# Performance work log

Hardware: AMD Instinct MI355X
Metric: run time of the kernel (lower is better)

Reference implementation:

```python
import jax, jax.numpy as jnp
import numpy as np

N_NODES = 100000
IN_CH = 128
HID = 256
EMB = 128
N_EDGES_GRAPH = 1000000
N_PAIRS = 500000
BN_EPS = 1e-5


def setup_inputs() -> dict:
    key = jax.random.key(0)
    ks = jax.random.split(key, 20)
    glorot = lambda k, fi, fo: jax.random.normal(k, (fi, fo), jnp.float32) * (1.0 / np.sqrt(fi))
    pair_dim = EMB * 4 + 2  # 514
    return {
        "x": jax.random.normal(ks[0], (N_NODES, IN_CH), jnp.float32),
        "edge_index": jax.random.randint(ks[1], (2, N_EDGES_GRAPH), 0, N_NODES, jnp.int64),
        "edge_pairs": jax.random.randint(ks[2], (N_PAIRS, 2), 0, N_NODES, jnp.int64),
        # normalizer buffers
        "x_mean": jnp.zeros((IN_CH,), jnp.float32),
        "x_std": jnp.ones((IN_CH,), jnp.float32),
        # log-degree buffer (as after set_degree)
        "log_degree": jax.random.uniform(ks[3], (N_NODES,), jnp.float32) * 5.0,
        # encoder: Linear(in,hid) -> BN(hid) -> ReLU -> Dropout -> Linear(hid,emb) -> ReLU
        "W1": glorot(ks[4], IN_CH, HID), "b1": jnp.zeros((HID,), jnp.float32),
        "bn_gamma": jnp.ones((HID,), jnp.float32), "bn_beta": jnp.zeros((HID,), jnp.float32),
        "bn_mean": jnp.zeros((HID,), jnp.float32), "bn_var": jnp.ones((HID,), jnp.float32),
        "W2": glorot(ks[5], HID, EMB), "b2": jnp.zeros((EMB,), jnp.float32),
        # scorer: Linear(514,256) -> ReLU -> Dropout -> Linear(256,128) -> ReLU -> Linear(128,1)
        "SW1": glorot(ks[6], pair_dim, HID), "Sb1": jnp.zeros((HID,), jnp.float32),
        "SW2": glorot(ks[7], HID, HID // 2), "Sb2": jnp.zeros((HID // 2,), jnp.float32),
        "SW3": glorot(ks[8], HID // 2, 1), "Sb3": jnp.zeros((1,), jnp.float32),
    }


def reference(x, edge_index, edge_pairs, x_mean, x_std, log_degree,
              W1, b1, bn_gamma, bn_beta, bn_mean, bn_var, W2, b2,
              SW1, Sb1, SW2, Sb2, SW3, Sb3):
    # ---- encode ----
    xf = jnp.nan_to_num(x, nan=0.0, posinf=0.0, neginf=0.0)
    xf = jnp.clip((xf - x_mean) / x_std, -10.0, 10.0)
    h = xf @ W1 + b1                                    # [N, HID]
    h = (h - bn_mean) * jax.lax.rsqrt(bn_var + BN_EPS) * bn_gamma + bn_beta  # BN (eval)
    h = jax.nn.relu(h)                                  # dropout = identity (eval)
    z = jax.nn.relu(h @ W2 + b2)                        # [N, EMB]
    # ---- score_from_embeddings ----
    si = edge_pairs[:, 0]
    di = edge_pairs[:, 1]
    src = z[si]                                         # [E, EMB]
    dst = z[di]
    deg_pair = jnp.stack([log_degree[si], log_degree[di]], axis=1)  # [E, 2]
    pair = jnp.concatenate([src, dst, src * dst, jnp.abs(src - dst), deg_pair], axis=1)  # [E, 4*EMB+2]
    s = jax.nn.relu(pair @ SW1 + Sb1)
    s = jax.nn.relu(s @ SW2 + Sb2)
    logits = (s @ SW3 + Sb3).reshape(-1)                # [E]
    return jnp.nan_to_num(logits, nan=0.0, posinf=20.0, neginf=-20.0)
```

## Files before the change

kernel.cpp:

```cpp
#include <hip/hip_runtime.h>
#include <hip/hip_bf16.h>
#include <math.h>

typedef unsigned short u16;
typedef __attribute__((ext_vector_type(8))) short bf16x8;
typedef __attribute__((ext_vector_type(8))) unsigned short u16x8;
typedef __attribute__((ext_vector_type(4))) float f32x4;
typedef __attribute__((ext_vector_type(4))) unsigned u32x4;
typedef __attribute__((ext_vector_type(2))) unsigned u32x2;

#define N_NODES 100000
#define IN_CH 128
#define HID 256
#define EMB 128
#define N_PAIRS 500000
#define BN_EPS 1e-5f

#define PBM 64

__device__ __forceinline__ u16 f2bf(float f) {
    unsigned u = __builtin_bit_cast(unsigned, f);
    unsigned r = u + 0x7FFFu + ((u >> 16) & 1u);
    return (u16)(r >> 16);
}
__device__ __forceinline__ float bf2f(u16 h) {
    unsigned u = ((unsigned)h) << 16;
    return __builtin_bit_cast(float, u);
}
__device__ __forceinline__ unsigned pk2(float a, float b) {
    __hip_bfloat162 h = __float22bfloat162_rn(make_float2(a, b));
    unsigned u;
    __builtin_memcpy(&u, &h, sizeof(u));
    return u;
}

__device__ __forceinline__ void store8(u16* buf, int base, const float* v) {
    u32x4 hv;
    #pragma unroll
    for (int q = 0; q < 4; ++q) hv[q] = pk2(v[2 * q], v[2 * q + 1]);
    *reinterpret_cast<u32x4*>(&buf[base]) = hv;
}

__global__ __launch_bounds__(256) void prep_weights(
    const float* __restrict__ SW1, const float* __restrict__ SW2,
    const float* __restrict__ W1,  const float* __restrict__ W2,
    u16* __restrict__ w1h, u16* __restrict__ w2h,
    u16* __restrict__ w1nh, u16* __restrict__ w1nl,
    u16* __restrict__ w2nh, u16* __restrict__ w2nl)
{
    const int tid = blockIdx.x * 256 + threadIdx.x;
    if (tid < 131072) {
        const int j = tid & 7, l = (tid >> 3) & 63, ks = (tid >> 9) & 15, mt = tid >> 13;
        const int n = mt * 16 + (l & 15);
        const int k = ks * 32 + ((l >> 4) << 3) + j;
        w1h[tid] = f2bf(SW1[(size_t)k * HID + n]);
    } else if (tid < 163840) {
        const int t2 = tid - 131072;
        const int j = t2 & 7, l = (t2 >> 3) & 63, ks = (t2 >> 9) & 7, mt = t2 >> 12;
        const int n = mt * 16 + (l & 15);
        const int k = ks * 32 + ((l >> 4) << 3) + j;
        w2h[t2] = f2bf(SW2[(size_t)k * (HID / 2) + n]);
    } else if (tid < 196608) {
        const int t3 = tid - 163840;
        const int j = t3 & 7, l = (t3 >> 3) & 63, ks = (t3 >> 9) & 3, mt = t3 >> 11;
        const int n = mt * 16 + (l & 15);
        const int k = ks * 32 + ((l >> 4) << 3) + j;
        const float v = W1[(size_t)k * HID + n];
        const u16 h = f2bf(v);
        w1nh[t3] = h;
        w1nl[t3] = f2bf(v - bf2f(h));
    } else if (tid < 229376) {
        const int t4 = tid - 196608;
        const int j = t4 & 7, l = (t4 >> 3) & 63, ks = (t4 >> 9) & 7, mt = t4 >> 12;
        const int n = mt * 16 + (l & 15);
        const int k = ks * 32 + ((l >> 4) << 3) + j;
        const float v = W2[(size_t)k * EMB + n];
        const u16 h = f2bf(v);
        w2nh[t4] = h;
        w2nl[t4] = f2bf(v - bf2f(h));
    }
}

__global__ __launch_bounds__(256) void node_mfma_kernel(
    const float* __restrict__ x,
    const float* __restrict__ x_mean, const float* __restrict__ x_std,
    const float* __restrict__ b1,
    const float* __restrict__ bn_gamma, const float* __restrict__ bn_beta,
    const float* __restrict__ bn_mean,  const float* __restrict__ bn_var,
    const float* __restrict__ b2,
    const u16* __restrict__ w1nh, const u16* __restrict__ w1nl,
    const u16* __restrict__ w2nh, const u16* __restrict__ w2nl,
    u16* __restrict__ z)
{
    __shared__ __align__(16) u16 XF[8192];
    __shared__ __align__(16) u16 HF[16384];

    const int t   = threadIdx.x;
    const int w   = t >> 6;
    const int l   = t & 63;
    const int l15 = l & 15;
    const int l4  = l >> 4;
    const int n0  = blockIdx.x * 64;
    const int nd  = (n0 + l < N_NODES) ? (n0 + l) : (N_NODES - 1);

    {
        const float* xp = x + (size_t)nd * IN_CH + w * 32;
        float v[32];
        #pragma unroll
        for (int q = 0; q < 8; ++q)
            *reinterpret_cast<float4*>(&v[q * 4]) = *reinterpret_cast<const float4*>(xp + q * 4);
        #pragma unroll
        for (int q = 0; q < 8; ++q) {
            float4 m4 = *reinterpret_cast<const float4*>(x_mean + w * 32 + q * 4);
            float4 s4 = *reinterpret_cast<const float4*>(x_std  + w * 32 + q * 4);
            float mm[4] = {m4.x, m4.y, m4.z, m4.w};
            float ss[4] = {s4.x, s4.y, s4.z, s4.w};
            #pragma unroll
            for (int e = 0; e < 4; ++e) {
                float val = v[q * 4 + e];
                if (!isfinite(val)) val = 0.0f;
                val = (val - mm[e]) / ss[e];
                v[q * 4 + e] = fminf(fmaxf(val, -10.0f), 10.0f);
            }
        }
        #pragma unroll
        for (int q = 0; q < 4; ++q) {
            const int base = (w * 4 + l4) * 512 + (l15 + 16 * q) * 8;
            store8(XF, base, &v[q * 8]);
        }
    }
    __syncthreads();

    f32x4 acc[4][4];
    #pragma unroll
    for (int m = 0; m < 4; ++m)
        #pragma unroll
        for (int nt = 0; nt < 4; ++nt) acc[m][nt] = (f32x4){0.f, 0.f, 0.f, 0.f};

    #pragma unroll
    for (int sl = 0; sl < 4; ++sl) {
        bf16x8 wh[4], wl[4];
        #pragma unroll
        for (int m = 0; m < 4; ++m) {
            const size_t bo = ((size_t)((w * 4 + m) * 4 + sl) * 64 + l) * 8;
            wh[m] = *reinterpret_cast<const bf16x8*>(&w1nh[bo]);
            wl[m] = *reinterpret_cast<const bf16x8*>(&w1nl[bo]);
        }
        bf16x8 fh[4];
        #pragma unroll
        for (int nt = 0; nt < 4; ++nt)
            fh[nt] = *reinterpret_cast<const bf16x8*>(&XF[(sl * 4 + nt) * 512 + l * 8]);
        __builtin_amdgcn_s_setprio(1);
        #pragma unroll
        for (int m = 0; m < 4; ++m)
            #pragma unroll
            for (int nt = 0; nt < 4; ++nt)
                acc[m][nt] = __builtin_amdgcn_mfma_f32_16x16x32_bf16(wh[m], fh[nt], acc[m][nt], 0, 0, 0);
        #pragma unroll
        for (int m = 0; m < 4; ++m)
            #pragma unroll
            for (int nt = 0; nt < 4; ++nt)
                acc[m][nt] = __builtin_amdgcn_mfma_f32_16x16x32_bf16(wl[m], fh[nt], acc[m][nt], 0, 0, 0);
        __builtin_amdgcn_s_setprio(0);
    }

    #pragma unroll
    for (int m = 0; m < 4; ++m) {
        const int mt = w * 4 + m;
        const int nb = mt * 16 + l4 * 4;
        float4 b1v = *reinterpret_cast<const float4*>(b1 + nb);
        float4 gv  = *reinterpret_cast<const float4*>(bn_gamma + nb);
        float4 bev = *reinterpret_cast<const float4*>(bn_beta + nb);
        float4 mev = *reinterpret_cast<const float4*>(bn_mean + nb);
        float4 vav = *reinterpret_cast<const float4*>(bn_var + nb);
        float scale[4], shift[4];
        float bb[4] = {b1v.x, b1v.y, b1v.z, b1v.w};
        float gg[4] = {gv.x, gv.y, gv.z, gv.w};
        float be[4] = {bev.x, bev.y, bev.z, bev.w};
        float me[4] = {mev.x, mev.y, mev.z, mev.w};
        float va[4] = {vav.x, vav.y, vav.z, vav.w};
        #pragma unroll
        for (int r = 0; r < 4; ++r) {
            scale[r] = gg[r] * rsqrtf(va[r] + BN_EPS);
            shift[r] = (bb[r] - me[r]) * scale[r] + be[r];
        }
        #pragma unroll
        for (int nt = 0; nt < 4; ++nt) {
            float v[4];
            #pragma unroll
            for (int r = 0; r < 4; ++r)
                v[r] = fmaxf(fmaf(acc[m][nt][r], scale[r], shift[r]), 0.0f);
            u32x2 hv;
            hv[0] = pk2(v[0], v[1]);
            hv[1] = pk2(v[2], v[3]);
            const int base = ((mt >> 1) * 4 + nt) * 512
                           + (l15 + 16 * ((mt & 1) * 2 + (l4 >> 1))) * 8
                           + (l4 & 1) * 4;
            *reinterpret_cast<u32x2*>(&HF[base]) = hv;
        }
    }
    __syncthreads();

    f32x4 acc2[2][4];
    #pragma unroll
    for (int m2 = 0; m2 < 2; ++m2)
        #pragma unroll
        for (int nt = 0; nt < 4; ++nt) acc2[m2][nt] = (f32x4){0.f, 0.f, 0.f, 0.f};

    #pragma unroll
    for (int ks2 = 0; ks2 < 8; ++ks2) {
        bf16x8 wh2[2], wl2[2];
        #pragma unroll
        for (int m2 = 0; m2 < 2; ++m2) {
            const size_t bo = ((size_t)((w * 2 + m2) * 8 + ks2) * 64 + l) * 8;
            wh2[m2] = *reinterpret_cast<const bf16x8*>(&w2nh[bo]);
            wl2[m2] = *reinterpret_cast<const bf16x8*>(&w2nl[bo]);
        }
        bf16x8 fh[4];
        #pragma unroll
        for (int nt = 0; nt < 4; ++nt)
            fh[nt] = *reinterpret_cast<const bf16x8*>(&HF[(ks2 * 4 + nt) * 512 + l * 8]);
        __builtin_amdgcn_s_setprio(1);
        #pragma unroll
        for (int m2 = 0; m2 < 2; ++m2)
            #pragma unroll
            for (int nt = 0; nt < 4; ++nt)
                acc2[m2][nt] = __builtin_amdgcn_mfma_f32_16x16x32_bf16(wh2[m2], fh[nt], acc2[m2][nt], 0, 0, 0);
        #pragma unroll
        for (int m2 = 0; m2 < 2; ++m2)
            #pragma unroll
            for (int nt = 0; nt < 4; ++nt)
                acc2[m2][nt] = __builtin_amdgcn_mfma_f32_16x16x32_bf16(wl2[m2], fh[nt], acc2[m2][nt], 0, 0, 0);
        __builtin_amdgcn_s_setprio(0);
    }

    #pragma unroll
    for (int m2 = 0; m2 < 2; ++m2) {
        const int nb2 = (w * 2 + m2) * 16 + l4 * 4;
        float4 b2v = *reinterpret_cast<const float4*>(b2 + nb2);
        float bb[4] = {b2v.x, b2v.y, b2v.z, b2v.w};
        #pragma unroll
        for (int nt = 0; nt < 4; ++nt) {
            const int node = n0 + nt * 16 + l15;
            if (node < N_NODES) {
                float v0 = fmaxf(acc2[m2][nt][0] + bb[0], 0.0f);
                float v1 = fmaxf(acc2[m2][nt][1] + bb[1], 0.0f);
                float v2 = fmaxf(acc2[m2][nt][2] + bb[2], 0.0f);
                float v3 = fmaxf(acc2[m2][nt][3] + bb[3], 0.0f);
                u32x2 hv;
                hv[0] = pk2(v0, v1);
                hv[1] = pk2(v2, v3);
                *reinterpret_cast<u32x2*>(z + (size_t)node * EMB + nb2) = hv;
            }
        }
    }
}

__global__ __launch_bounds__(256) void pair_mfma_kernel(
    const u16* __restrict__ z,
    const int* __restrict__ pairs,
    const float* __restrict__ logdeg,
    const u16* __restrict__ w1h,
    const u16* __restrict__ w2h,
    const float* __restrict__ SW1, const float* __restrict__ Sb1,
    const float* __restrict__ Sb2,
    const float* __restrict__ SW3, const float* __restrict__ Sb3,
    float* __restrict__ out)
{
    __shared__ __align__(16) u16 F0[8192];
    __shared__ __align__(16) u16 F1[8192];
    __shared__ __align__(16) u16 F2[8192];
    __shared__ __align__(16) u16 F3[8192];
    __shared__ float red[4][4][16];

    const int t   = threadIdx.x;
    const int w   = t >> 6;
    const int l   = t & 63;
    const int l15 = l & 15;
    const int l4  = l >> 4;
    const int p0  = blockIdx.x * PBM;

    const int qb  = (w & 1) * 2;
    const int bS0 = (((w >> 1)) * 4 + l4) * 512 + (l15 + 16 * (qb + 0)) * 8;
    const int bS1 = (((w >> 1)) * 4 + l4) * 512 + (l15 + 16 * (qb + 1)) * 8;
    const int bD0 = ((2 + (w >> 1)) * 4 + l4) * 512 + (l15 + 16 * (qb + 0)) * 8;
    const int bD1 = ((2 + (w >> 1)) * 4 + l4) * 512 + (l15 + 16 * (qb + 1)) * 8;

    const int gp  = (p0 + l < N_PAIRS) ? (p0 + l) : (N_PAIRS - 1);
    const int gsi = pairs[(size_t)gp * 2 + 0];
    const int gdi = pairs[(size_t)gp * 2 + 1];

    const u16* zs0 = z + (size_t)gsi * EMB + w * 16;
    const u16* zd0 = z + (size_t)gdi * EMB + w * 16;
    u16x8 s00 = *reinterpret_cast<const u16x8*>(zs0);
    u16x8 s01 = *reinterpret_cast<const u16x8*>(zs0 + 8);
    u16x8 d00 = *reinterpret_cast<const u16x8*>(zd0);
    u16x8 d01 = *reinterpret_cast<const u16x8*>(zd0 + 8);
    u16x8 s10 = *reinterpret_cast<const u16x8*>(zs0 + 64);
    u16x8 s11 = *reinterpret_cast<const u16x8*>(zs0 + 72);
    u16x8 d10 = *reinterpret_cast<const u16x8*>(zd0 + 64);
    u16x8 d11 = *reinterpret_cast<const u16x8*>(zd0 + 72);

    auto rebuildR = [&](u16x8 sa, u16x8 sb, u16x8 da, u16x8 db, float* pv, float* av) {
        #pragma unroll
        for (int qq = 0; qq < 8; ++qq) {
            const float s = bf2f(sa[qq]);
            const float d = bf2f(da[qq]);
            pv[qq] = s * d;
            av[qq] = fabsf(s - d);
        }
        #pragma unroll
        for (int qq = 0; qq < 8; ++qq) {
            const float s = bf2f(sb[qq]);
            const float d = bf2f(db[qq]);
            pv[8 + qq] = s * d;
            av[8 + qq] = fabsf(s - d);
        }
    };

    *reinterpret_cast<u16x8*>(&F0[bS0]) = s00;
    *reinterpret_cast<u16x8*>(&F0[bS1]) = s01;
    *reinterpret_cast<u16x8*>(&F0[bD0]) = d00;
    *reinterpret_cast<u16x8*>(&F0[bD1]) = d01;
    *reinterpret_cast<u16x8*>(&F1[bS0]) = s10;
    *reinterpret_cast<u16x8*>(&F1[bS1]) = s11;
    *reinterpret_cast<u16x8*>(&F1[bD0]) = d10;
    *reinterpret_cast<u16x8*>(&F1[bD1]) = d11;
    {
        float pv[16], av[16];
        rebuildR(s00, s01, d00, d01, pv, av);
        store8(F2, bS0, pv + 0);
        store8(F2, bS1, pv + 8);
        store8(F2, bD0, av + 0);
        store8(F2, bD1, av + 8);
        rebuildR(s10, s11, d10, d11, pv, av);
        store8(F3, bS0, pv + 0);
        store8(F3, bS1, pv + 8);
        store8(F3, bD0, av + 0);
        store8(F3, bD1, av + 8);
    }

    float ldS[4], ldD[4];
    #pragma unroll
    for (int nt = 0; nt < 4; ++nt) {
        const int pidx = (p0 + nt * 16 + l15 < N_PAIRS) ? (p0 + nt * 16 + l15) : (N_PAIRS - 1);
        ldS[nt] = logdeg[pairs[(size_t)pidx * 2 + 0]];
        ldD[nt] = logdeg[pairs[(size_t)pidx * 2 + 1]];
    }

    __syncthreads();

    f32x4 acc[4][4];
    #pragma unroll
    for (int m = 0; m < 4; ++m)
        #pragma unroll
        for (int nt = 0; nt < 4; ++nt) acc[m][nt] = (f32x4){0.f, 0.f, 0.f, 0.f};

    auto run_pass = [&](const u16* buf, int k0, int k1, int k2, int k3) {
        const int ksg[4] = {k0, k1, k2, k3};
        bf16x8 wh[2][4];
        #pragma unroll
        for (int m = 0; m < 4; ++m) {
            const size_t bo = ((size_t)((w * 4 + m) * 16 + ksg[0]) * 64 + l) * 8;
            wh[0][m] = *reinterpret_cast<const bf16x8*>(&w1h[bo]);
        }
        #pragma unroll
        for (int sl = 0; sl < 4; ++sl) {
            const int cur = sl & 1;
            if (sl < 3) {
                #pragma unroll
                for (int m = 0; m < 4; ++m) {
                    const size_t bo = ((size_t)((w * 4 + m) * 16 + ksg[sl + 1]) * 64 + l) * 8;
                    wh[cur ^ 1][m] = *reinterpret_cast<const bf16x8*>(&w1h[bo]);
                }
            }
            #pragma unroll
            for (int nh = 0; nh < 2; ++nh) {
                bf16x8 fh[2];
                #pragma unroll
                for (int e = 0; e < 2; ++e)
                    fh[e] = *reinterpret_cast<const bf16x8*>(&buf[(sl * 4 + nh * 2 + e) * 512 + l * 8]);
                __builtin_amdgcn_s_setprio(1);
                #pragma unroll
                for (int m = 0; m < 4; ++m)
                    #pragma unroll
                    for (int e = 0; e < 2; ++e)
                        acc[m][nh * 2 + e] = __builtin_amdgcn_mfma_f32_16x16x32_bf16(wh[cur][m], fh[e], acc[m][nh * 2 + e], 0, 0, 0);
                __builtin_amdgcn_s_setprio(0);
            }
        }
    };

    run_pass(F0, 0, 1, 4, 5);
    run_pass(F2, 8, 9, 12, 13);
    run_pass(F1, 2, 3, 6, 7);
    run_pass(F3, 10, 11, 14, 15);
    __syncthreads();

    f32x4 acc2[2][4];
    #pragma unroll
    for (int m2 = 0; m2 < 2; ++m2)
        #pragma unroll
        for (int nt = 0; nt < 4; ++nt) acc2[m2][nt] = (f32x4){0.f, 0.f, 0.f, 0.f};

    auto epi1 = [&](u16* buf, int g) {
        #pragma unroll
        for (int mm = 0; mm < 2; ++mm) {
            const int m  = 2 * g + mm;
            const int mt = w * 4 + m;
            const int nb = mt * 16 + l4 * 4;
            float sb[4], wa[4], wb[4];
            *reinterpret_cast<float4*>(sb) = *reinterpret_cast<const float4*>(&Sb1[nb]);
            *reinterpret_cast<float4*>(wa) = *reinterpret_cast<const float4*>(&SW1[(size_t)512 * HID + nb]);
            *reinterpret_cast<float4*>(wb) = *reinterpret_cast<const float4*>(&SW1[(size_t)513 * HID + nb]);
            #pragma unroll
            for (int nt = 0; nt < 4; ++nt) {
                float v[4];
                #pragma unroll
                for (int r = 0; r < 4; ++r) {
                    float x0 = acc[m][nt][r] + sb[r];
                    x0 = fmaf(ldS[nt], wa[r], x0);
                    x0 = fmaf(ldD[nt], wb[r], x0);
                    v[r] = fmaxf(x0, 0.0f);
                }
                u32x2 hv;
                hv[0] = pk2(v[0], v[1]);
                hv[1] = pk2(v[2], v[3]);
                const int base = (w * 4 + nt) * 512
                               + (l15 + 16 * ((m & 1) * 2 + (l4 >> 1))) * 8
                               + (l4 & 1) * 4;
                *reinterpret_cast<u32x2*>(&buf[base]) = hv;
            }
        }
    };

    auto mfma2 = [&](const u16* buf, int g) {
        #pragma unroll
        for (int cs = 0; cs < 4; ++cs) {
            const int ks2 = cs * 2 + g;
            bf16x8 wh2[2];
            #pragma unroll
            for (int m2 = 0; m2 < 2; ++m2) {
                const size_t bo = ((size_t)((w * 2 + m2) * 8 + ks2) * 64 + l) * 8;
                wh2[m2] = *reinterpret_cast<const bf16x8*>(&w2h[bo]);
            }
            #pragma unroll
            for (int nh = 0; nh < 2; ++nh) {
                bf16x8 fh[2];
                #pragma unroll
                for (int e = 0; e < 2; ++e)
                    fh[e] = *reinterpret_cast<const bf16x8*>(&buf[(cs * 4 + nh * 2 + e) * 512 + l * 8]);
                __builtin_amdgcn_s_setprio(1);
                #pragma unroll
                for (int m2 = 0; m2 < 2; ++m2)
                    #pragma unroll
                    for (int e = 0; e < 2; ++e)
                        acc2[m2][nh * 2 + e] = __builtin_amdgcn_mfma_f32_16x16x32_bf16(wh2[m2], fh[e], acc2[m2][nh * 2 + e], 0, 0, 0);
                __builtin_amdgcn_s_setprio(0);
            }
        }
    };

    epi1(F0, 0);
    __syncthreads();
    epi1(F1, 1);
    mfma2(F0, 0);
    __syncthreads();
    mfma2(F1, 1);

    {
        float part[4] = {0.f, 0.f, 0.f, 0.f};
        #pragma unroll
        for (int m2 = 0; m2 < 2; ++m2) {
            const int nb2 = (w * 2 + m2) * 16 + l4 * 4;
            float sb[4], w3[4];
            *reinterpret_cast<float4*>(sb) = *reinterpret_cast<const float4*>(&Sb2[nb2]);
            *reinterpret_cast<float4*>(w3) = *reinterpret_cast<const float4*>(&SW3[nb2]);
            #pragma unroll
            for (int nt = 0; nt < 4; ++nt)
                #pragma unroll
                for (int r = 0; r < 4; ++r)
                    part[nt] = fmaf(fmaxf(acc2[m2][nt][r] + sb[r], 0.0f), w3[r], part[nt]);
        }
        #pragma unroll
        for (int nt = 0; nt < 4; ++nt) {
            part[nt] += __shfl_xor(part[nt], 16);
            part[nt] += __shfl_xor(part[nt], 32);
        }
        if (l < 16) {
            #pragma unroll
            for (int nt = 0; nt < 4; ++nt) red[w][nt][l15] = part[nt];
        }
    }
    __syncthreads();

    if (t < 64) {
        const int nt = t >> 4, pp = t & 15;
        float v = red[0][nt][pp] + red[1][nt][pp] + red[2][nt][pp] + red[3][nt][pp] + Sb3[0];
        if (isnan(v)) v = 0.0f;
        else if (isinf(v)) v = (v > 0.0f) ? 20.0f : -20.0f;
        const int pidx = p0 + nt * 16 + pp;
        if (pidx < N_PAIRS) out[pidx] = v;
    }
}

extern "C" void kernel_launch(void* const* d_in, const int* in_sizes, int n_in,
                              void* d_out, int out_size, void* d_ws, size_t ws_size,
                              hipStream_t stream)
{
    const float* x        = (const float*)d_in[0];
    const int*   pairs    = (const int*)d_in[2];
    const float* x_mean   = (const float*)d_in[3];
    const float* x_std    = (const float*)d_in[4];
    const float* logdeg   = (const float*)d_in[5];
    const float* W1       = (const float*)d_in[6];
    const float* b1       = (const float*)d_in[7];
    const float* bn_gamma = (const float*)d_in[8];
    const float* bn_beta  = (const float*)d_in[9];
    const float* bn_mean  = (const float*)d_in[10];
    const float* bn_var   = (const float*)d_in[11];
    const float* W2       = (const float*)d_in[12];
    const float* b2       = (const float*)d_in[13];
    const float* SW1      = (const float*)d_in[14];
    const float* Sb1      = (const float*)d_in[15];
    const float* SW2      = (const float*)d_in[16];
    const float* Sb2      = (const float*)d_in[17];
    const float* SW3      = (const float*)d_in[18];
    const float* Sb3      = (const float*)d_in[19];

    float* outp = (float*)d_out;

    char* wsb = (char*)d_ws;
    u16* zbuf = (u16*)wsb;
    u16* w1h  = (u16*)(wsb + 25600000);
    u16* w2h  = (u16*)(wsb + 25862144);
    u16* w1nh = (u16*)(wsb + 25927680);
    u16* w1nl = (u16*)(wsb + 25993216);
    u16* w2nh = (u16*)(wsb + 26058752);
    u16* w2nl = (u16*)(wsb + 26124288);

    prep_weights<<<896, 256, 0, stream>>>(SW1, SW2, W1, W2,
                                          w1h, w2h,
                                          w1nh, w1nl, w2nh, w2nl);

    node_mfma_kernel<<<(N_NODES + 63) / 64, 256, 0, stream>>>(
        x, x_mean, x_std, b1, bn_gamma, bn_beta, bn_mean, bn_var, b2,
        w1nh, w1nl, w2nh, w2nl, zbuf);

    pair_mfma_kernel<<<(N_PAIRS + PBM - 1) / PBM, 256, 0, stream>>>(
        zbuf, pairs, logdeg, w1h, w2h, SW1, Sb1, Sb2, SW3, Sb3, outp);
}
```

Measured before the change: 248.0 us.

## Switch scorer first layer to 32x32x16 MFMA tiles with matching layouts

Replaces the 16x16x32 bf16 MFMA tiling of the first scorer layer with 32x32x16 MFMA. The SW1 prepacking, the LDS feature layout, the log-degree loads and the epilogue write-back are all remapped to the 32-wide fragment layout. The larger tiles mean fewer MFMA instructions and fewer weight and feature fragment loads per FLOP. The cost is bigger accumulator vectors and more complex index mapping, which raises register pressure and the risk of layout bugs.

```diff
diff --git a/kernel.cpp b/kernel.cpp
--- a/kernel.cpp
+++ b/kernel.cpp
@@ -6,6 +6,7 @@
 typedef __attribute__((ext_vector_type(8))) short bf16x8;
 typedef __attribute__((ext_vector_type(8))) unsigned short u16x8;
 typedef __attribute__((ext_vector_type(4))) float f32x4;
+typedef __attribute__((ext_vector_type(16))) float f32x16;
 typedef __attribute__((ext_vector_type(4))) unsigned u32x4;
 typedef __attribute__((ext_vector_type(2))) unsigned u32x2;
 
@@ -50,9 +51,9 @@
 {
     const int tid = blockIdx.x * 256 + threadIdx.x;
     if (tid < 131072) {
-        const int j = tid & 7, l = (tid >> 3) & 63, ks = (tid >> 9) & 15, mt = tid >> 13;
-        const int n = mt * 16 + (l & 15);
-        const int k = ks * 32 + ((l >> 4) << 3) + j;
+        const int j = tid & 7, l = (tid >> 3) & 63, ks16 = (tid >> 9) & 31, mt32 = tid >> 14;
+        const int n = mt32 * 32 + (l & 31);
+        const int k = ks16 * 16 + ((l >> 5) << 3) + j;
         w1h[tid] = f2bf(SW1[(size_t)k * HID + n]);
     } else if (tid < 163840) {
         const int t2 = tid - 131072;
@@ -278,13 +279,15 @@
     const int l   = t & 63;
     const int l15 = l & 15;
     const int l4  = l >> 4;
+    const int hi5 = l >> 5;
+    const int l31 = l & 31;
     const int p0  = blockIdx.x * PBM;
 
-    const int qb  = (w & 1) * 2;
-    const int bS0 = (((w >> 1)) * 4 + l4) * 512 + (l15 + 16 * (qb + 0)) * 8;
-    const int bS1 = (((w >> 1)) * 4 + l4) * 512 + (l15 + 16 * (qb + 1)) * 8;
-    const int bD0 = ((2 + (w >> 1)) * 4 + l4) * 512 + (l15 + 16 * (qb + 0)) * 8;
-    const int bD1 = ((2 + (w >> 1)) * 4 + l4) * 512 + (l15 + 16 * (qb + 1)) * 8;
+    const int nw  = l >> 5;
+    const int sB0 = ((w * 2 + nw) * 64 + l31) * 8;
+    const int sB1 = sB0 + 32 * 8;
+    const int dB0 = (((4 + w) * 2 + nw) * 64 + l31) * 8;
+    const int dB1 = dB0 + 32 * 8;
 
     const int gp  = (p0 + l < N_PAIRS) ? (p0 + l) : (N_PAIRS - 1);
     const int gsi = pairs[(size_t)gp * 2 + 0];
@@ -318,83 +321,82 @@
         }
     };
 
-    *reinterpret_cast<u16x8*>(&F0[bS0]) = s00;
-    *reinterpret_cast<u16x8*>(&F0[bS1]) = s01;
-    *reinterpret_cast<u16x8*>(&F0[bD0]) = d00;
-    *reinterpret_cast<u16x8*>(&F0[bD1]) = d01;
-    *reinterpret_cast<u16x8*>(&F1[bS0]) = s10;
-    *reinterpret_cast<u16x8*>(&F1[bS1]) = s11;
-    *reinterpret_cast<u16x8*>(&F1[bD0]) = d10;
-    *reinterpret_cast<u16x8*>(&F1[bD1]) = d11;
+    *reinterpret_cast<u16x8*>(&F0[sB0]) = s00;
+    *reinterpret_cast<u16x8*>(&F0[sB1]) = s01;
+    *reinterpret_cast<u16x8*>(&F0[dB0]) = d00;
+    *reinterpret_cast<u16x8*>(&F0[dB1]) = d01;
+    *reinterpret_cast<u16x8*>(&F1[sB0]) = s10;
+    *reinterpret_cast<u16x8*>(&F1[sB1]) = s11;
+    *reinterpret_cast<u16x8*>(&F1[dB0]) = d10;
+    *reinterpret_cast<u16x8*>(&F1[dB1]) = d11;
     {
         float pv[16], av[16];
         rebuildR(s00, s01, d00, d01, pv, av);
-        store8(F2, bS0, pv + 0);
-        store8(F2, bS1, pv + 8);
-        store8(F2, bD0, av + 0);
-        store8(F2, bD1, av + 8);
+        store8(F2, sB0, pv + 0);
+        store8(F2, sB1, pv + 8);
+        store8(F2, dB0, av + 0);
+        store8(F2, dB1, av + 8);
         rebuildR(s10, s11, d10, d11, pv, av);
-        store8(F3, bS0, pv + 0);
-        store8(F3, bS1, pv + 8);
-        store8(F3, bD0, av + 0);
-        store8(F3, bD1, av + 8);
-    }
-
-    float ldS[4], ldD[4];
-    #pragma unroll
-    for (int nt = 0; nt < 4; ++nt) {
-        const int pidx = (p0 + nt * 16 + l15 < N_PAIRS) ? (p0 + nt * 16 + l15) : (N_PAIRS - 1);
-        ldS[nt] = logdeg[pairs[(size_t)pidx * 2 + 0]];
-        ldD[nt] = logdeg[pairs[(size_t)pidx * 2 + 1]];
-    }
-
-    __syncthreads();
-
-    f32x4 acc[4][4];
-    #pragma unroll
-    for (int m = 0; m < 4; ++m)
-        #pragma unroll
-        for (int nt = 0; nt < 4; ++nt) acc[m][nt] = (f32x4){0.f, 0.f, 0.f, 0.f};
-
-    auto run_pass = [&](const u16* buf, int k0, int k1, int k2, int k3) {
-        const int ksg[4] = {k0, k1, k2, k3};
-        bf16x8 wh[2][4];
-        #pragma unroll
-        for (int m = 0; m < 4; ++m) {
-            const size_t bo = ((size_t)((w * 4 + m) * 16 + ksg[0]) * 64 + l) * 8;
-            wh[0][m] = *reinterpret_cast<const bf16x8*>(&w1h[bo]);
-        }
-        #pragma unroll
-        for (int sl = 0; sl < 4; ++sl) {
-            const int cur = sl & 1;
-            if (sl < 3) {
+        store8(F3, sB0, pv + 0);
+        store8(F3, sB1, pv + 8);
+        store8(F3, dB0, av + 0);
+        store8(F3, dB1, av + 8);
+    }
+
+    float ldS2[2], ldD2[2];
+    #pragma unroll
+    for (int g2 = 0; g2 < 2; ++g2) {
+        const int pidx = (p0 + g2 * 32 + l31 < N_PAIRS) ? (p0 + g2 * 32 + l31) : (N_PAIRS - 1);
+        ldS2[g2] = logdeg[pairs[(size_t)pidx * 2 + 0]];
+        ldD2[g2] = logdeg[pairs[(size_t)pidx * 2 + 1]];
+    }
+
+    __syncthreads();
+
+    f32x16 acc32[2][2];
+    #pragma unroll
+    for (int mi = 0; mi < 2; ++mi)
+        #pragma unroll
+        for (int nt = 0; nt < 2; ++nt)
+            #pragma unroll
+            for (int r = 0; r < 16; ++r) acc32[mi][nt][r] = 0.0f;
+
+    auto run_pass32 = [&](const u16* buf, int kA, int kB) {
+        bf16x8 wh[2][2];
+        #pragma unroll
+        for (int mi = 0; mi < 2; ++mi) {
+            const size_t bo = ((size_t)((2 * w + mi) * 32 + kA) * 64 + l) * 8;
+            wh[0][mi] = *reinterpret_cast<const bf16x8*>(&w1h[bo]);
+        }
+        #pragma unroll
+        for (int ksl = 0; ksl < 8; ++ksl) {
+            const int cur = ksl & 1;
+            if (ksl < 7) {
+                const int gks = (ksl + 1 < 4) ? (kA + ksl + 1) : (kB + ksl - 3);
                 #pragma unroll
-                for (int m = 0; m < 4; ++m) {
-                    const size_t bo = ((size_t)((w * 4 + m) * 16 + ksg[sl + 1]) * 64 + l) * 8;
-                    wh[cur ^ 1][m] = *reinterpret_cast<const bf16x8*>(&w1h[bo]);
+                for (int mi = 0; mi < 2; ++mi) {
+                    const size_t bo = ((size_t)((2 * w + mi) * 32 + gks) * 64 + l) * 8;
+                    wh[cur ^ 1][mi] = *reinterpret_cast<const bf16x8*>(&w1h[bo]);
                 }
             }
-            #pragma unroll
-            for (int nh = 0; nh < 2; ++nh) {
-                bf16x8 fh[2];
+            bf16x8 fh[2];
+            #pragma unroll
+            for (int nt = 0; nt < 2; ++nt)
+                fh[nt] = *reinterpret_cast<const bf16x8*>(&buf[((ksl * 2 + nt) * 64 + l) * 8]);
+            __builtin_amdgcn_s_setprio(1);
+            #pragma unroll
+            for (int mi = 0; mi < 2; ++mi)
                 #pragma unroll
-                for (int e = 0; e < 2; ++e)
-                    fh[e] = *reinterpret_cast<const bf16x8*>(&buf[(sl * 4 + nh * 2 + e) * 512 + l * 8]);
-                __builtin_amdgcn_s_setprio(1);
-                #pragma unroll
-                for (int m = 0; m < 4; ++m)
-                    #pragma unroll
-                    for (int e = 0; e < 2; ++e)
-                        acc[m][nh * 2 + e] = __builtin_amdgcn_mfma_f32_16x16x32_bf16(wh[cur][m], fh[e], acc[m][nh * 2 + e], 0, 0, 0);
-                __builtin_amdgcn_s_setprio(0);
-            }
+                for (int nt = 0; nt < 2; ++nt)
+                    acc32[mi][nt] = __builtin_amdgcn_mfma_f32_32x32x16_bf16(wh[cur][mi], fh[nt], acc32[mi][nt], 0, 0, 0);
+            __builtin_amdgcn_s_setprio(0);
         }
     };
 
-    run_pass(F0, 0, 1, 4, 5);
-    run_pass(F2, 8, 9, 12, 13);
-    run_pass(F1, 2, 3, 6, 7);
-    run_pass(F3, 10, 11, 14, 15);
+    run_pass32(F0, 0, 8);
+    run_pass32(F2, 16, 24);
+    run_pass32(F1, 4, 12);
+    run_pass32(F3, 20, 28);
     __syncthreads();
 
     f32x4 acc2[2][4];
@@ -403,32 +405,32 @@
         #pragma unroll
         for (int nt = 0; nt < 4; ++nt) acc2[m2][nt] = (f32x4){0.f, 0.f, 0.f, 0.f};
 
-    auto epi1 = [&](u16* buf, int g) {
-        #pragma unroll
-        for (int mm = 0; mm < 2; ++mm) {
-            const int m  = 2 * g + mm;
-            const int mt = w * 4 + m;
-            const int nb = mt * 16 + l4 * 4;
-            float sb[4], wa[4], wb[4];
-            *reinterpret_cast<float4*>(sb) = *reinterpret_cast<const float4*>(&Sb1[nb]);
-            *reinterpret_cast<float4*>(wa) = *reinterpret_cast<const float4*>(&SW1[(size_t)512 * HID + nb]);
-            *reinterpret_cast<float4*>(wb) = *reinterpret_cast<const float4*>(&SW1[(size_t)513 * HID + nb]);
-            #pragma unroll
-            for (int nt = 0; nt < 4; ++nt) {
+    auto epi1_32 = [&](u16* buf, int mi) {
+        const int mt32 = 2 * w + mi;
+        #pragma unroll
+        for (int nt = 0; nt < 2; ++nt) {
+            const float lS = ldS2[nt];
+            const float lD = ldD2[nt];
+            const int nt2 = nt * 2 + ((l >> 4) & 1);
+            #pragma unroll
+            for (int q = 0; q < 4; ++q) {
+                const int nb = mt32 * 32 + 8 * q + 4 * hi5;
+                float sb[4], wa[4], wb[4];
+                *reinterpret_cast<float4*>(sb) = *reinterpret_cast<const float4*>(&Sb1[nb]);
+                *reinterpret_cast<float4*>(wa) = *reinterpret_cast<const float4*>(&SW1[(size_t)512 * HID + nb]);
+                *reinterpret_cast<float4*>(wb) = *reinterpret_cast<const float4*>(&SW1[(size_t)513 * HID + nb]);
                 float v[4];
                 #pragma unroll
-                for (int r = 0; r < 4; ++r) {
-                    float x0 = acc[m][nt][r] + sb[r];
-                    x0 = fmaf(ldS[nt], wa[r], x0);
-                    x0 = fmaf(ldD[nt], wb[r], x0);
-                    v[r] = fmaxf(x0, 0.0f);
+                for (int rr = 0; rr < 4; ++rr) {
+                    float x0 = acc32[mi][nt][q * 4 + rr] + sb[rr];
+                    x0 = fmaf(lS, wa[rr], x0);
+                    x0 = fmaf(lD, wb[rr], x0);
+                    v[rr] = fmaxf(x0, 0.0f);
                 }
                 u32x2 hv;
                 hv[0] = pk2(v[0], v[1]);
                 hv[1] = pk2(v[2], v[3]);
-                const int base = (w * 4 + nt) * 512
-                               + (l15 + 16 * ((m & 1) * 2 + (l4 >> 1))) * 8
-                               + (l4 & 1) * 4;
+                const int base = (w * 4 + nt2) * 512 + (l15 + 16 * q) * 8 + 4 * hi5;
                 *reinterpret_cast<u32x2*>(&buf[base]) = hv;
             }
         }
@@ -461,9 +463,9 @@
         }
     };
 
-    epi1(F0, 0);
-    __syncthreads();
-    epi1(F1, 1);
+    epi1_32(F0, 0);
+    __syncthreads();
+    epi1_32(F1, 1);
     mfma2(F0, 0);
     __syncthreads();
     mfma2(F1, 1);
```

Result: slower. 297.7 us (+20.0%).
